# Kernel optimization log

Measured on AMD Instinct MI355X. Metric: run time of the kernel, lower is better.

The kernel has to match this reference:

```python
import jax, jax.numpy as jnp
import numpy as np

DT = 1e-3
STEPS = 128
UNITS_OSC = 512
MLP_UNITS = [1024, 512, 256]
ACTION_DIM = 256
BATCH = 64


def setup_inputs() -> dict:
    key = jax.random.key(0)
    ks = jax.random.split(key, 16)
    inp = {
        "z": jax.random.normal(ks[0], (BATCH, 2 * UNITS_OSC), dtype=jnp.float32),
        "omega": jax.random.uniform(ks[1], (BATCH, 1), dtype=jnp.float32),
        "b": jax.random.uniform(ks[2], (BATCH, UNITS_OSC), dtype=jnp.float32),
    }
    dims = [UNITS_OSC] + MLP_UNITS
    i = 3
    for l, (din, dout) in enumerate(zip(dims[:-1], dims[1:])):
        scale = 1.0 / np.sqrt(din)
        inp[f"W{l}_re"] = (jax.random.normal(ks[i], (din, dout), dtype=jnp.float32) * scale); i += 1
        inp[f"W{l}_im"] = (jax.random.normal(ks[i], (din, dout), dtype=jnp.float32) * scale); i += 1
        inp[f"b{l}_re"] = jnp.zeros((dout,), dtype=jnp.float32)
        inp[f"b{l}_im"] = jnp.zeros((dout,), dtype=jnp.float32)
    return inp


def _hopf(z, omega, b):
    # z: (B, 2*U) = [real | imag]; Hopf dynamics with harmonic frequencies k*omega
    x, y = z[:, :UNITS_OSC], z[:, UNITS_OSC:]
    r2 = x * x + y * y
    w = omega * jnp.arange(1, UNITS_OSC + 1, dtype=z.dtype)  # (B, U)
    dx = (b - r2) * x - w * y
    dy = (b - r2) * y + w * x
    return jnp.concatenate([x + DT * dx, y + DT * dy], axis=-1)


def _complex_mlp(z, params):
    # complex dense stack: (xr+i*yi) @ (Wr+i*Wi) + (br+i*bi), tanh on re/im parts
    x, y = jnp.split(z, 2, axis=-1)
    for (Wr, Wi, br, bi) in params:
        xr = x @ Wr - y @ Wi + br
        yi = x @ Wi + y @ Wr + bi
        x, y = jnp.tanh(xr), jnp.tanh(yi)
    return jnp.concatenate([x, y], axis=-1)


def reference(z, omega, b,
              W0_re, W0_im, b0_re, b0_im,
              W1_re, W1_im, b1_re, b1_im,
              W2_re, W2_im, b2_re, b2_im):
    params = [(W0_re, W0_im, b0_re, b0_im),
              (W1_re, W1_im, b1_re, b1_im),
              (W2_re, W2_im, b2_re, b2_im)]
    # first oscillator step (done before the while_loop in the original)
    z1 = _hopf(z, omega, b)
    o0 = _complex_mlp(z1, params)

    def step(zc, _):
        zn = _hopf(zc, omega, b)
        return zn, _complex_mlp(zn, params)

    _, outs = jax.lax.scan(step, z1, None, length=STEPS - 1)  # (STEPS-1, B, 2*A)
    outs = jnp.concatenate([o0[None], outs], axis=0)          # (STEPS, B, 2*A)
    out = jnp.transpose(outs, (1, 0, 2))[:, :, :ACTION_DIM]   # (B, STEPS, A)
    return out, z1
```

## Files before the change

kernel.cpp:

```cpp
#include <hip/hip_runtime.h>
#include <hip/hip_bf16.h>
#include <stdint.h>

#define AS1 __attribute__((address_space(1)))
#define AS3 __attribute__((address_space(3)))

typedef __bf16 bf16x8 __attribute__((ext_vector_type(8)));
typedef float f32x4 __attribute__((ext_vector_type(4)));

__device__ __forceinline__ float fast_tanh(float x) {
    float e = __expf(2.0f * x);
    return 1.0f - 2.0f / (e + 1.0f);
}

__device__ __forceinline__ float ldin(const void* p, int idx, int f32) {
    return f32 ? ((const float*)p)[idx]
               : __bfloat162float(((const __hip_bfloat16*)p)[idx]);
}

__device__ __forceinline__ unsigned short f2bf(float v) {
    __hip_bfloat16 h = __float2bfloat16(v);
    return *(unsigned short*)&h;
}

__device__ __forceinline__ void gload_lds16(const __hip_bfloat16* g, AS3 char* l) {
    __builtin_amdgcn_global_load_lds((AS1 void*)g, (AS3 void*)l, 16, 0, 0);
}

__global__ void detect_dtype(const unsigned short* __restrict__ z, int* __restrict__ flag)
{
    const int l = threadIdx.x;
    int c = 0;
    for (int i = l; i < 512; i += 64)
        c += (((z[i] >> 7) & 0xFF) >= 0xC8) ? 1 : 0;
#pragma unroll
    for (int off = 32; off; off >>= 1) c += __shfl_down(c, off);
    if (l == 0) *flag = (c > 8) ? 1 : 0;
}

__global__ __launch_bounds__(256)
void hopf_traj(const void* __restrict__ z, const void* __restrict__ omega,
               const void* __restrict__ bc, const int* __restrict__ flag,
               __hip_bfloat16* __restrict__ Z, char* __restrict__ dout)
{
    const int f32 = *flag;
    const int tid = blockIdx.x * 256 + threadIdx.x;
    const int b = tid >> 9;
    const int i = tid & 511;
    float x = ldin(z, b * 1024 + i, f32);
    float y = ldin(z, b * 1024 + 512 + i, f32);
    const float om = ldin(omega, b, f32);
    const float bb = ldin(bc, b * 512 + i, f32);
    const float w  = om * (float)(i + 1);
    __hip_bfloat16* zt = Z + b * 1024 + i;
    for (int t = 0; t < 128; ++t) {
        const float r2 = x * x + y * y;
        const float f  = bb - r2;
        const float dx = f * x - w * y;
        const float dy = f * y + w * x;
        x += 0.001f * dx;
        y += 0.001f * dy;
        zt[t * 65536]       = __float2bfloat16(x);
        zt[t * 65536 + 512] = __float2bfloat16(y);
        if (t == 0) {
            if (f32) {
                float* o = (float*)(dout + (size_t)2097152 * 4);
                o[b * 1024 + i] = x; o[b * 1024 + 512 + i] = y;
            } else {
                __hip_bfloat16* o = (__hip_bfloat16*)(dout + (size_t)2097152 * 2);
                o[b * 1024 + i] = __float2bfloat16(x);
                o[b * 1024 + 512 + i] = __float2bfloat16(y);
            }
        }
    }
}

__global__ __launch_bounds__(256)
void prep_fused(const void* __restrict__ W0r, const void* __restrict__ W0i,
                const void* __restrict__ W1r, const void* __restrict__ W1i,
                const void* __restrict__ W2r, const void* __restrict__ W2i,
                const void* __restrict__ b0r, const void* __restrict__ b0i,
                const void* __restrict__ b1r, const void* __restrict__ b1i,
                const void* __restrict__ b2r, const int* __restrict__ flag,
                __hip_bfloat16* __restrict__ WT0, __hip_bfloat16* __restrict__ WT1,
                __hip_bfloat16* __restrict__ WT2, float* __restrict__ biasOut)
{
    const int bid = blockIdx.x;
    const int t   = threadIdx.x;
    const int f32 = *flag;

    if (bid >= 1088) {
        const int idx = (bid - 1088) * 256 + t;
        float v;
        if      (idx < 1024) v = ldin(b0r, idx, f32);
        else if (idx < 2048) v = ldin(b0i, idx - 1024, f32);
        else if (idx < 2560) v = ldin(b1r, idx - 2048, f32);
        else if (idx < 3072) v = ldin(b1i, idx - 2560, f32);
        else                 v = ldin(b2r, idx - 3072, f32);
        biasOut[idx] = v;
        return;
    }

    __shared__ float T[64][65];

    int din, dout, KT, nt, kt;
    const void *Wr, *Wi;
    __hip_bfloat16* dst;
    if (bid < 512)       { din = 512;  dout = 1024; KT = 1024; Wr = W0r; Wi = W0i; dst = WT0;
                           nt = bid >> 4;            kt = bid & 15; }
    else if (bid < 1024) { din = 1024; dout = 512;  KT = 2048; Wr = W1r; Wi = W1i; dst = WT1;
                           nt = (bid - 512) >> 5;    kt = (bid - 512) & 31; }
    else                 { din = 512;  dout = 256;  KT = 1024; Wr = W2r; Wi = W2i; dst = WT2;
                           nt = (bid - 1024) >> 4;   kt = (bid - 1024) & 15; }

    const int n0 = nt * 64, k0 = kt * 64;
    const void* src; float sg; int col0, krel;
    if (n0 < dout) {
        col0 = n0;
        if (k0 < din) { src = Wr; sg =  1.f; krel = k0; }
        else          { src = Wi; sg = -1.f; krel = k0 - din; }
    } else {
        col0 = n0 - dout;
        if (k0 < din) { src = Wi; sg =  1.f; krel = k0; }
        else          { src = Wr; sg =  1.f; krel = k0 - din; }
    }

    const int lr = t >> 4;
    const int lc = t & 15;
#pragma unroll
    for (int p = 0; p < 4; ++p) {
        const int r = p * 16 + lr;
        const int c = lc * 4;
        const size_t gi = (size_t)(krel + r) * dout + col0 + c;
        float v0, v1, v2, v3;
        if (f32) {
            float4 v = *(const float4*)((const float*)src + gi);
            v0 = v.x; v1 = v.y; v2 = v.z; v3 = v.w;
        } else {
            ushort4 u = *(const ushort4*)((const unsigned short*)src + gi);
            __hip_bfloat16 h0, h1, h2, h3;
            *(unsigned short*)&h0 = u.x; *(unsigned short*)&h1 = u.y;
            *(unsigned short*)&h2 = u.z; *(unsigned short*)&h3 = u.w;
            v0 = __bfloat162float(h0); v1 = __bfloat162float(h1);
            v2 = __bfloat162float(h2); v3 = __bfloat162float(h3);
        }
        T[r][c] = sg * v0; T[r][c + 1] = sg * v1;
        T[r][c + 2] = sg * v2; T[r][c + 3] = sg * v3;
    }
    __syncthreads();
#pragma unroll
    for (int q = 0; q < 4; ++q) {
        const int n = q * 16 + lr;
        const int k8 = lc;
        ushort4 u;
        u.x = f2bf(T[k8 * 4 + 0][n]); u.y = f2bf(T[k8 * 4 + 1][n]);
        u.z = f2bf(T[k8 * 4 + 2][n]); u.w = f2bf(T[k8 * 4 + 3][n]);
        *(ushort4*)((unsigned short*)dst + (size_t)(n0 + n) * KT + k0 + k8 * 4) = u;
    }
}

template<int MT, int MODE>
__global__ __launch_bounds__(256)
void gemm_bias_tanh(const __hip_bfloat16* __restrict__ A,
                    const __hip_bfloat16* __restrict__ Bt,
                    const float* __restrict__ bias,
                    void* __restrict__ Cv, const int* __restrict__ flag,
                    int M, int N, int K)
{
    constexpr int AI = MT / 32;
    __shared__ __align__(16) __hip_bfloat16 As[MT * 64];
    __shared__ __align__(16) __hip_bfloat16 Bs[128 * 64];

    const int tid = threadIdx.x, lane = tid & 63, w = tid >> 6;
    const int wx = w & 1, wy = w >> 1;
    const int m0 = blockIdx.y * MT;
    const int n0 = blockIdx.x * 128;

    const int sl = lane & 7, lr8 = lane >> 3;
    const __hip_bfloat16* gA[AI];
    const __hip_bfloat16* gB[4];
#pragma unroll
    for (int p = 0; p < AI; ++p) {
        const int row = w * (MT / 4) + p * 8 + lr8;
        const int q = sl ^ (row & 7);
        gA[p] = A + (size_t)(m0 + row) * K + q * 8;
    }
#pragma unroll
    for (int p = 0; p < 4; ++p) {
        const int row = w * 32 + p * 8 + lr8;
        const int q = sl ^ (row & 7);
        gB[p] = Bt + (size_t)(n0 + row) * K + q * 8;
    }
    AS3 char* lA = (AS3 char*)As + w * (MT * 32);
    AS3 char* lB = (AS3 char*)Bs + w * 4096;

    const int fr = lane & 15, fq = lane >> 4;
    const int swz = (fq ^ (fr & 7)) * 8;
    const int arow = wy * (MT / 2) + fr;
    const int brow = wx * 64 + fr;

    f32x4 acc[AI][4];
#pragma unroll
    for (int i = 0; i < AI; ++i)
#pragma unroll
        for (int j = 0; j < 4; ++j)
            acc[i][j] = (f32x4){0.f, 0.f, 0.f, 0.f};

    const int NKT = K >> 6;
    for (int kt = 0; kt < NKT; ++kt) {
        const int kk = kt << 6;
#pragma unroll
        for (int p = 0; p < AI; ++p) gload_lds16(gA[p] + kk, lA + p * 1024);
#pragma unroll
        for (int p = 0; p < 4; ++p)  gload_lds16(gB[p] + kk, lB + p * 1024);
        __syncthreads();
#pragma unroll
        for (int ks = 0; ks < 2; ++ks) {
            const int so = swz ^ (ks << 5);
            bf16x8 af[AI], bv[4];
#pragma unroll
            for (int i = 0; i < AI; ++i)
                af[i] = *(const bf16x8*)(As + (arow + i * 16) * 64 + so);
#pragma unroll
            for (int j = 0; j < 4; ++j)
                bv[j] = *(const bf16x8*)(Bs + (brow + j * 16) * 64 + so);
#pragma unroll
            for (int i = 0; i < AI; ++i)
#pragma unroll
                for (int j = 0; j < 4; ++j)
                    acc[i][j] = __builtin_amdgcn_mfma_f32_16x16x32_bf16(af[i], bv[j], acc[i][j], 0, 0, 0);
        }
        __syncthreads();
    }

    const int col_l = lane & 15;
    const int rq    = lane >> 4;
    const int f32   = (MODE == 1) ? *flag : 0;
    float bvv[4];
#pragma unroll
    for (int j = 0; j < 4; ++j)
        bvv[j] = bias[n0 + wx * 64 + j * 16 + col_l];

#pragma unroll
    for (int i = 0; i < AI; ++i) {
#pragma unroll
        for (int j = 0; j < 4; ++j) {
            const int gc = n0 + wx * 64 + j * 16 + col_l;
#pragma unroll
            for (int r = 0; r < 4; ++r) {
                const int gr = m0 + wy * (MT / 2) + i * 16 + rq * 4 + r;
                const float v = fast_tanh(acc[i][j][r] + bvv[j]);
                if (MODE == 0) {
                    ((__hip_bfloat16*)Cv)[(size_t)gr * (size_t)N + gc] = __float2bfloat16(v);
                } else {
                    const size_t idx = (size_t)(gr & 63) * 32768 + (size_t)(gr >> 6) * 256 + (size_t)gc;
                    if (f32) ((float*)Cv)[idx] = v;
                    else     ((__hip_bfloat16*)Cv)[idx] = __float2bfloat16(v);
                }
            }
        }
    }
}

extern "C" void kernel_launch(void* const* d_in, const int* in_sizes, int n_in,
                              void* d_out, int out_size, void* d_ws, size_t ws_size,
                              hipStream_t stream)
{
    (void)in_sizes; (void)n_in; (void)out_size; (void)ws_size;
    char* ws = (char*)d_ws;
    __hip_bfloat16* Z    = (__hip_bfloat16*)(ws);
    __hip_bfloat16* H0   = (__hip_bfloat16*)(ws + (16u << 20));
    __hip_bfloat16* WT0  = (__hip_bfloat16*)(ws + (48u << 20));
    __hip_bfloat16* WT1  = (__hip_bfloat16*)(ws + (52u << 20));
    __hip_bfloat16* WT2  = (__hip_bfloat16*)(ws + (56u << 20));
    float*          bias = (float*)        (ws + (56u << 20) + (512u << 10));
    int*            flag = (int*)          (ws + (57u << 20));

    detect_dtype<<<1, 64, 0, stream>>>((const unsigned short*)d_in[0], flag);
    hopf_traj<<<128, 256, 0, stream>>>(d_in[0], d_in[1], d_in[2], flag, Z, (char*)d_out);
    prep_fused<<<1101, 256, 0, stream>>>(d_in[3], d_in[4], d_in[7], d_in[8], d_in[11], d_in[12],
                                         d_in[5], d_in[6], d_in[9], d_in[10], d_in[13], flag,
                                         WT0, WT1, WT2, bias);

    gemm_bias_tanh<128, 0><<<dim3(16, 64), 256, 0, stream>>>(Z, WT0, bias, H0, flag, 8192, 2048, 1024);
    gemm_bias_tanh<128, 0><<<dim3(8, 64), 256, 0, stream>>>(H0, WT1, bias + 2048, Z, flag, 8192, 1024, 2048);
    gemm_bias_tanh<64, 1><<<dim3(2, 128), 256, 0, stream>>>(Z, WT2, bias + 3072, d_out, flag, 8192, 256, 1024);
}
```

Measured before the change: 219.1 us.

## Fuse setup kernels and remap GEMM tiles across XCDs

Merges dtype detection, the Hopf trajectory and weight/bias preparation into one launch, with every block detecting the dtype itself through a shared atomic counter. This removes two kernel launches and the serial dependency on the flag. The GEMMs move to a 1D grid whose block-to-tile mapping groups N tiles per XCD to improve L2 reuse of weights. The second GEMM switches to 64-row M tiles, doubling its block count. The costs are redundant per-block dtype detection and smaller tiles that may lower MFMA efficiency.

```diff
diff --git a/kernel.cpp b/kernel.cpp
--- a/kernel.cpp
+++ b/kernel.cpp
@@ -27,70 +27,72 @@
     __builtin_amdgcn_global_load_lds((AS1 void*)g, (AS3 void*)l, 16, 0, 0);
 }
 
-__global__ void detect_dtype(const unsigned short* __restrict__ z, int* __restrict__ flag)
+__global__ __launch_bounds__(256)
+void setup_all(const void* __restrict__ z, const void* __restrict__ omega,
+               const void* __restrict__ bc,
+               const void* __restrict__ W0r, const void* __restrict__ W0i,
+               const void* __restrict__ W1r, const void* __restrict__ W1i,
+               const void* __restrict__ W2r, const void* __restrict__ W2i,
+               const void* __restrict__ b0r, const void* __restrict__ b0i,
+               const void* __restrict__ b1r, const void* __restrict__ b1i,
+               const void* __restrict__ b2r,
+               __hip_bfloat16* __restrict__ Z, __hip_bfloat16* __restrict__ WT0,
+               __hip_bfloat16* __restrict__ WT1, __hip_bfloat16* __restrict__ WT2,
+               float* __restrict__ biasOut, int* __restrict__ flagOut,
+               char* __restrict__ dout)
 {
-    const int l = threadIdx.x;
-    int c = 0;
-    for (int i = l; i < 512; i += 64)
-        c += (((z[i] >> 7) & 0xFF) >= 0xC8) ? 1 : 0;
-#pragma unroll
-    for (int off = 32; off; off >>= 1) c += __shfl_down(c, off);
-    if (l == 0) *flag = (c > 8) ? 1 : 0;
-}
-
-__global__ __launch_bounds__(256)
-void hopf_traj(const void* __restrict__ z, const void* __restrict__ omega,
-               const void* __restrict__ bc, const int* __restrict__ flag,
-               __hip_bfloat16* __restrict__ Z, char* __restrict__ dout)
-{
-    const int f32 = *flag;
-    const int tid = blockIdx.x * 256 + threadIdx.x;
-    const int b = tid >> 9;
-    const int i = tid & 511;
-    float x = ldin(z, b * 1024 + i, f32);
-    float y = ldin(z, b * 1024 + 512 + i, f32);
-    const float om = ldin(omega, b, f32);
-    const float bb = ldin(bc, b * 512 + i, f32);
-    const float w  = om * (float)(i + 1);
-    __hip_bfloat16* zt = Z + b * 1024 + i;
-    for (int t = 0; t < 128; ++t) {
-        const float r2 = x * x + y * y;
-        const float f  = bb - r2;
-        const float dx = f * x - w * y;
-        const float dy = f * y + w * x;
-        x += 0.001f * dx;
-        y += 0.001f * dy;
-        zt[t * 65536]       = __float2bfloat16(x);
-        zt[t * 65536 + 512] = __float2bfloat16(y);
-        if (t == 0) {
-            if (f32) {
-                float* o = (float*)(dout + (size_t)2097152 * 4);
-                o[b * 1024 + i] = x; o[b * 1024 + 512 + i] = y;
-            } else {
-                __hip_bfloat16* o = (__hip_bfloat16*)(dout + (size_t)2097152 * 2);
-                o[b * 1024 + i] = __float2bfloat16(x);
-                o[b * 1024 + 512 + i] = __float2bfloat16(y);
+    __shared__ float T[64][65];
+    __shared__ int sflag;
+    const int t   = threadIdx.x;
+    const int bid = blockIdx.x;
+
+    if (t == 0) sflag = 0;
+    __syncthreads();
+    {
+        const unsigned short* zz = (const unsigned short*)z;
+        const int c = ((((zz[t] >> 7) & 0xFF) >= 0xC8) ? 1 : 0)
+                    + ((((zz[t + 256] >> 7) & 0xFF) >= 0xC8) ? 1 : 0);
+        if (c) atomicAdd(&sflag, c);
+    }
+    __syncthreads();
+    const int f32 = (sflag > 8) ? 1 : 0;
+
+    if (bid < 128) {
+        const int tid = bid * 256 + t;
+        const int b = tid >> 9;
+        const int i = tid & 511;
+        float x = ldin(z, b * 1024 + i, f32);
+        float y = ldin(z, b * 1024 + 512 + i, f32);
+        const float om = ldin(omega, b, f32);
+        const float bb = ldin(bc, b * 512 + i, f32);
+        const float w  = om * (float)(i + 1);
+        __hip_bfloat16* zt = Z + b * 1024 + i;
+        for (int s = 0; s < 128; ++s) {
+            const float r2 = x * x + y * y;
+            const float f  = bb - r2;
+            const float dx = f * x - w * y;
+            const float dy = f * y + w * x;
+            x += 0.001f * dx;
+            y += 0.001f * dy;
+            zt[s * 65536]       = __float2bfloat16(x);
+            zt[s * 65536 + 512] = __float2bfloat16(y);
+            if (s == 0) {
+                if (f32) {
+                    float* o = (float*)(dout + (size_t)2097152 * 4);
+                    o[b * 1024 + i] = x; o[b * 1024 + 512 + i] = y;
+                } else {
+                    __hip_bfloat16* o = (__hip_bfloat16*)(dout + (size_t)2097152 * 2);
+                    o[b * 1024 + i] = __float2bfloat16(x);
+                    o[b * 1024 + 512 + i] = __float2bfloat16(y);
+                }
             }
         }
-    }
-}
-
-__global__ __launch_bounds__(256)
-void prep_fused(const void* __restrict__ W0r, const void* __restrict__ W0i,
-                const void* __restrict__ W1r, const void* __restrict__ W1i,
-                const void* __restrict__ W2r, const void* __restrict__ W2i,
-                const void* __restrict__ b0r, const void* __restrict__ b0i,
-                const void* __restrict__ b1r, const void* __restrict__ b1i,
-                const void* __restrict__ b2r, const int* __restrict__ flag,
-                __hip_bfloat16* __restrict__ WT0, __hip_bfloat16* __restrict__ WT1,
-                __hip_bfloat16* __restrict__ WT2, float* __restrict__ biasOut)
-{
-    const int bid = blockIdx.x;
-    const int t   = threadIdx.x;
-    const int f32 = *flag;
-
-    if (bid >= 1088) {
-        const int idx = (bid - 1088) * 256 + t;
+        return;
+    }
+
+    if (bid >= 1216) {
+        if (bid == 1216 && t == 0) *flagOut = f32;
+        const int idx = (bid - 1216) * 256 + t;
         float v;
         if      (idx < 1024) v = ldin(b0r, idx, f32);
         else if (idx < 2048) v = ldin(b0i, idx - 1024, f32);
@@ -101,26 +103,25 @@
         return;
     }
 
-    __shared__ float T[64][65];
-
-    int din, dout, KT, nt, kt;
+    const int wbid = bid - 128;
+    int din, dout_, KT, nt, kt;
     const void *Wr, *Wi;
     __hip_bfloat16* dst;
-    if (bid < 512)       { din = 512;  dout = 1024; KT = 1024; Wr = W0r; Wi = W0i; dst = WT0;
-                           nt = bid >> 4;            kt = bid & 15; }
-    else if (bid < 1024) { din = 1024; dout = 512;  KT = 2048; Wr = W1r; Wi = W1i; dst = WT1;
-                           nt = (bid - 512) >> 5;    kt = (bid - 512) & 31; }
-    else                 { din = 512;  dout = 256;  KT = 1024; Wr = W2r; Wi = W2i; dst = WT2;
-                           nt = (bid - 1024) >> 4;   kt = (bid - 1024) & 15; }
+    if (wbid < 512)       { din = 512;  dout_ = 1024; KT = 1024; Wr = W0r; Wi = W0i; dst = WT0;
+                            nt = wbid >> 4;           kt = wbid & 15; }
+    else if (wbid < 1024) { din = 1024; dout_ = 512;  KT = 2048; Wr = W1r; Wi = W1i; dst = WT1;
+                            nt = (wbid - 512) >> 5;   kt = (wbid - 512) & 31; }
+    else                  { din = 512;  dout_ = 256;  KT = 1024; Wr = W2r; Wi = W2i; dst = WT2;
+                            nt = (wbid - 1024) >> 4;  kt = (wbid - 1024) & 15; }
 
     const int n0 = nt * 64, k0 = kt * 64;
     const void* src; float sg; int col0, krel;
-    if (n0 < dout) {
+    if (n0 < dout_) {
         col0 = n0;
         if (k0 < din) { src = Wr; sg =  1.f; krel = k0; }
         else          { src = Wi; sg = -1.f; krel = k0 - din; }
     } else {
-        col0 = n0 - dout;
+        col0 = n0 - dout_;
         if (k0 < din) { src = Wi; sg =  1.f; krel = k0; }
         else          { src = Wr; sg =  1.f; krel = k0 - din; }
     }
@@ -131,7 +132,7 @@
     for (int p = 0; p < 4; ++p) {
         const int r = p * 16 + lr;
         const int c = lc * 4;
-        const size_t gi = (size_t)(krel + r) * dout + col0 + c;
+        const size_t gi = (size_t)(krel + r) * dout_ + col0 + c;
         float v0, v1, v2, v3;
         if (f32) {
             float4 v = *(const float4*)((const float*)src + gi);
@@ -159,7 +160,7 @@
     }
 }
 
-template<int MT, int MODE>
+template<int MT, int GX, int MODE>
 __global__ __launch_bounds__(256)
 void gemm_bias_tanh(const __hip_bfloat16* __restrict__ A,
                     const __hip_bfloat16* __restrict__ Bt,
@@ -173,8 +174,20 @@
 
     const int tid = threadIdx.x, lane = tid & 63, w = tid >> 6;
     const int wx = w & 1, wy = w >> 1;
-    const int m0 = blockIdx.y * MT;
-    const int n0 = blockIdx.x * 128;
+
+    constexpr int XG = GX >> 3;
+    int nt, mt;
+    const int bid = blockIdx.x;
+    if constexpr (XG > 0) {
+        const int xcd = bid & 7, r = bid >> 3;
+        nt = xcd * XG + (r % XG);
+        mt = r / XG;
+    } else {
+        nt = bid % GX;
+        mt = bid / GX;
+    }
+    const int m0 = mt * MT;
+    const int n0 = nt * 128;
 
     const int sl = lane & 7, lr8 = lane >> 3;
     const __hip_bfloat16* gA[AI];
@@ -207,8 +220,8 @@
             acc[i][j] = (f32x4){0.f, 0.f, 0.f, 0.f};
 
     const int NKT = K >> 6;
-    for (int kt = 0; kt < NKT; ++kt) {
-        const int kk = kt << 6;
+    for (int kt2 = 0; kt2 < NKT; ++kt2) {
+        const int kk = kt2 << 6;
 #pragma unroll
         for (int p = 0; p < AI; ++p) gload_lds16(gA[p] + kk, lA + p * 1024);
 #pragma unroll
@@ -276,13 +289,12 @@
     float*          bias = (float*)        (ws + (56u << 20) + (512u << 10));
     int*            flag = (int*)          (ws + (57u << 20));
 
-    detect_dtype<<<1, 64, 0, stream>>>((const unsigned short*)d_in[0], flag);
-    hopf_traj<<<128, 256, 0, stream>>>(d_in[0], d_in[1], d_in[2], flag, Z, (char*)d_out);
-    prep_fused<<<1101, 256, 0, stream>>>(d_in[3], d_in[4], d_in[7], d_in[8], d_in[11], d_in[12],
-                                         d_in[5], d_in[6], d_in[9], d_in[10], d_in[13], flag,
-                                         WT0, WT1, WT2, bias);
-
-    gemm_bias_tanh<128, 0><<<dim3(16, 64), 256, 0, stream>>>(Z, WT0, bias, H0, flag, 8192, 2048, 1024);
-    gemm_bias_tanh<128, 0><<<dim3(8, 64), 256, 0, stream>>>(H0, WT1, bias + 2048, Z, flag, 8192, 1024, 2048);
-    gemm_bias_tanh<64, 1><<<dim3(2, 128), 256, 0, stream>>>(Z, WT2, bias + 3072, d_out, flag, 8192, 256, 1024);
-}
+    setup_all<<<1229, 256, 0, stream>>>(d_in[0], d_in[1], d_in[2],
+                                        d_in[3], d_in[4], d_in[7], d_in[8], d_in[11], d_in[12],
+                                        d_in[5], d_in[6], d_in[9], d_in[10], d_in[13],
+                                        Z, WT0, WT1, WT2, bias, flag, (char*)d_out);
+
+    gemm_bias_tanh<128, 16, 0><<<1024, 256, 0, stream>>>(Z, WT0, bias, H0, flag, 8192, 2048, 1024);
+    gemm_bias_tanh<64, 8, 0><<<1024, 256, 0, stream>>>(H0, WT1, bias + 2048, Z, flag, 8192, 1024, 2048);
+    gemm_bias_tanh<64, 2, 1><<<256, 256, 0, stream>>>(Z, WT2, bias + 3072, d_out, flag, 8192, 256, 1024);
+}
```

New measurement: 210.9 us. -3.7%, faster.
